# Kernel tuning notes

Measured on AMD Instinct MI355X. Metric: run time of the kernel, lower is better.

The kernel has to match this reference:

```python
import jax, jax.numpy as jnp
import numpy as np

N_NODES = 100000
N_EDGES = 600000
H = 128          # hidden_units
LH = 256         # lin_hidden_units
F_IN = 3         # num_features (x, y, area)
C = 8            # out_classes


def setup_inputs() -> dict:
    key = jax.random.key(0)
    ks = jax.random.split(key, 12)
    s = 0.05
    return {
        "x": jax.random.normal(ks[0], (N_NODES, F_IN), dtype=jnp.float32),
        "edge_index": jax.random.randint(ks[1], (2, N_EDGES), 0, N_NODES, dtype=jnp.int64),
        # conv1: lin_l (aggregated neighbors, has bias), lin_r (root, no bias)
        "Wl1": jax.random.normal(ks[2], (H, F_IN), dtype=jnp.float32) * s,
        "bl1": jnp.zeros((H,), dtype=jnp.float32),
        "Wr1": jax.random.normal(ks[3], (H, F_IN), dtype=jnp.float32) * s,
        # conv2
        "Wl2": jax.random.normal(ks[4], (H, H), dtype=jnp.float32) * s,
        "bl2": jnp.zeros((H,), dtype=jnp.float32),
        "Wr2": jax.random.normal(ks[5], (H, H), dtype=jnp.float32) * s,
        # MLP head
        "W1": jax.random.normal(ks[6], (LH, H), dtype=jnp.float32) * s,
        "b1": jnp.zeros((LH,), dtype=jnp.float32),
        "W2": jax.random.normal(ks[7], (C, LH), dtype=jnp.float32) * s,
        "b2": jnp.zeros((C,), dtype=jnp.float32),
    }


def _normalize(x):
    coords = x[:, :2]                      # [N, 2]
    areas = x[:, 2:3]                      # [N, 1]
    mx = jnp.max(coords, axis=0)
    mn = jnp.min(coords, axis=0)
    theta = jnp.float32(np.pi / 2)
    c, sn = jnp.cos(theta), jnp.sin(theta)
    R = jnp.array([[1.0, 0.0], [0.0, 1.0]], dtype=x.dtype) * c + \
        jnp.array([[0.0, -1.0], [1.0, 0.0]], dtype=x.dtype) * sn
    rotated = coords @ R.T                 # (R @ coords.T).T
    rotate = (mx[1] - mn[1]) > (mx[0] - mn[0])
    coords = jnp.where(rotate, rotated, coords)
    coords = (coords - jnp.mean(coords, axis=0)) / jnp.max(coords, axis=0)
    areas = areas / jnp.max(areas, axis=0)
    return jnp.concatenate([coords, areas], axis=-1)


def _sage_conv(x, src, dst, Wl, bl, Wr):
    # mean aggregation of source features at target nodes
    msg = x[src]                                               # [E, d] gather
    agg = jax.ops.segment_sum(msg, dst, num_segments=N_NODES)  # [N, d]
    deg = jax.ops.segment_sum(jnp.ones((src.shape[0],), x.dtype), dst,
                              num_segments=N_NODES)
    agg = agg / jnp.maximum(deg, 1.0)[:, None]
    return agg @ Wl.T + bl + x @ Wr.T


def reference(x, edge_index, Wl1, bl1, Wr1, Wl2, bl2, Wr2, W1, b1, W2, b2):
    src, dst = edge_index[0], edge_index[1]
    h = _normalize(x)
    h = jnp.tanh(_sage_conv(h, src, dst, Wl1, bl1, Wr1))
    h = jnp.tanh(_sage_conv(h, src, dst, Wl2, bl2, Wr2))
    h = jnp.tanh(h @ W1.T + b1)
    h = h @ W2.T + b2
    return jax.nn.softmax(h, axis=1)
```

## Files before the change

kernel.cpp:

```cpp
#include <hip/hip_runtime.h>
#include <hip/hip_bf16.h>
#include <math.h>

#define N_NODES 100000
#define N_EDGES 600000
#define H 128
#define LH 256
#define CDIM 8
#define NB_STATS 256
#define NT128 ((N_NODES + 127) / 128)
#define ELLW 64
#define NB_NODE ((N_NODES + 255) / 256)

#define NBUCK 391
#define NBLK_P1 64
#define EPB (N_EDGES / NBLK_P1)
#define CAP 72

typedef __attribute__((ext_vector_type(8))) short short8;
typedef __attribute__((ext_vector_type(4))) float floatx4;

#define OFF_PART   0
#define OFF_DEG    2816
#define OFF_H0     (OFF_DEG + N_NODES)
#define OFF_ELL    (OFF_H0 + N_NODES*4)
#define OFF_CNTT   (OFF_ELL + N_NODES*ELLW)
#define OFF_SCR    (OFF_CNTT + NBUCK*NBLK_P1)
#define OFF_WPK2   (OFF_SCR + NBUCK*NBLK_P1*CAP*2)
#define OFF_WPK1   (OFF_WPK2 + 16384)
#define OFF_W2PK   (OFF_WPK1 + 16384)
#define OFF_XB     (OFF_W2PK + 2048)

__device__ __forceinline__ float rot_c() { return cosf(1.57079632679489661923f); }
__device__ __forceinline__ float rot_s() { return sinf(1.57079632679489661923f); }
__device__ __forceinline__ float bfhi(unsigned v) { return __uint_as_float(v & 0xffff0000u); }
__device__ __forceinline__ float bflo(unsigned v) { return __uint_as_float(v << 16); }
__device__ __forceinline__ unsigned short bfu(float f) {
    __hip_bfloat16 h = __float2bfloat16(f);
    return *(unsigned short*)&h;
}
__device__ __forceinline__ float ftanh(float x) {
    float e = __expf(2.0f * x);
    return 1.0f - 2.0f * __builtin_amdgcn_rcpf(e + 1.0f);
}

__global__ __launch_bounds__(256) void statsPart_k(const float* __restrict__ x,
        float* __restrict__ part, const int* __restrict__ ei,
        int* __restrict__ cntT, int2* __restrict__ scratch) {
    __shared__ float red[4][11];
    __shared__ int lcnt[NBUCK];
    int tid = threadIdx.x;

    if (blockIdx.x >= NB_STATS) {
        int blk = blockIdx.x - NB_STATS;
        for (int i = tid; i < NBUCK; i += 256) lcnt[i] = 0;
        __syncthreads();
        int base = blk * EPB;
        for (int e = base + tid; e < base + EPB; e += 256) {
            int s = ei[e], d = ei[N_EDGES + e];
            int b = d >> 8;
            int pos = atomicAdd(&lcnt[b], 1);
            scratch[(b * NBLK_P1 + blk) * CAP + pos] = make_int2(s, d);
        }
        __syncthreads();
        for (int i = tid; i < NBUCK; i += 256)
            cntT[i * NBLK_P1 + blk] = lcnt[i];
        return;
    }

    const float c = rot_c(), sn = rot_s();
    float mn0 = INFINITY, mx0 = -INFINITY, mn1 = INFINITY, mx1 = -INFINITY;
    float s0 = 0.f, s1 = 0.f, sr0 = 0.f, sr1 = 0.f;
    float mxr0 = -INFINITY, mxr1 = -INFINITY, mxa = -INFINITY;
    for (int i = blockIdx.x * 256 + tid; i < N_NODES; i += NB_STATS * 256) {
        float x0 = x[3*i], x1 = x[3*i+1], a = x[3*i+2];
        float r0 = c*x0 - sn*x1;
        float r1 = sn*x0 + c*x1;
        mn0 = fminf(mn0, x0); mx0 = fmaxf(mx0, x0);
        mn1 = fminf(mn1, x1); mx1 = fmaxf(mx1, x1);
        s0 += x0; s1 += x1; sr0 += r0; sr1 += r1;
        mxr0 = fmaxf(mxr0, r0); mxr1 = fmaxf(mxr1, r1);
        mxa = fmaxf(mxa, a);
    }
    float vals[11] = {mn0, mx0, mn1, mx1, s0, s1, sr0, sr1, mxr0, mxr1, mxa};
    int lane = tid & 63, wave = tid >> 6;
    #pragma unroll
    for (int v = 0; v < 11; v++) {
        const int op = (v==0||v==2) ? 0 : (v>=4 && v<=7) ? 2 : 1;
        float val = vals[v];
        #pragma unroll
        for (int off = 32; off > 0; off >>= 1) {
            float o = __shfl_down(val, off);
            val = (op==0) ? fminf(val,o) : (op==1) ? fmaxf(val,o) : (val+o);
        }
        if (lane == 0) red[wave][v] = val;
    }
    __syncthreads();
    if (tid < 11) {
        int v = tid;
        int op = (v==0||v==2) ? 0 : (v>=4 && v<=7) ? 2 : 1;
        float a = red[0][v], b = red[1][v], cc = red[2][v], d = red[3][v];
        float r = (op==0) ? fminf(fminf(a,b), fminf(cc,d))
                : (op==1) ? fmaxf(fmaxf(a,b), fmaxf(cc,d))
                : (a + b + cc + d);
        part[blockIdx.x * 11 + v] = r;
    }
}

__global__ __launch_bounds__(256) void binNorm_k(const float* __restrict__ x,
        const float* __restrict__ part, float4* __restrict__ h0,
        const float* __restrict__ Wl2, const float* __restrict__ Wr2,
        const float* __restrict__ W1, const float* __restrict__ W2,
        __hip_bfloat16* __restrict__ Wpk2, __hip_bfloat16* __restrict__ Wpk1,
        __hip_bfloat16* __restrict__ W2pk,
        const int* __restrict__ cntT, const int2* __restrict__ scratch,
        int* __restrict__ ell, int* __restrict__ deg) {
    __shared__ int pref[NBLK_P1 + 1];
    __shared__ int ncnt[256];
    __shared__ float res[11];
    int tid = threadIdx.x;

    if (blockIdx.x < NBUCK) {
        int b = blockIdx.x;
        ncnt[tid] = 0;
        if (tid < NBLK_P1) pref[tid + 1] = cntT[b * NBLK_P1 + tid];
        __syncthreads();
        if (tid == 0) {
            pref[0] = 0;
            int acc = 0;
            #pragma unroll 8
            for (int j = 0; j < NBLK_P1; j++) { acc += pref[j+1]; pref[j+1] = acc; }
        }
        __syncthreads();
        int T = pref[NBLK_P1];
        for (int f = tid; f < T; f += 256) {
            int lo = 0, hi = NBLK_P1;
            while (hi - lo > 1) {
                int mid = (lo + hi) >> 1;
                if (pref[mid] <= f) lo = mid; else hi = mid;
            }
            int2 sd = scratch[(b * NBLK_P1 + lo) * CAP + (f - pref[lo])];
            int pos = atomicAdd(&ncnt[sd.y & 255], 1);
            ell[(sd.y << 6) + pos] = sd.x;
        }
        __syncthreads();
        int n = (b << 8) + tid;
        if (n < N_NODES) deg[n] = ncnt[tid];
        return;
    }

    int nb = blockIdx.x - NBUCK;
    int i = nb * 256 + tid;
    if (tid < 64) {
        const int ops[11] = {0,1,0,1,2,2,2,2,1,1,1};
        for (int v = 0; v < 11; v++) {
            float val = part[tid * 11 + v];
            #pragma unroll
            for (int p = 1; p < 4; p++) {
                float o = part[(tid + p*64) * 11 + v];
                val = (ops[v]==0) ? fminf(val,o) : (ops[v]==1) ? fmaxf(val,o) : (val+o);
            }
            #pragma unroll
            for (int off = 32; off > 0; off >>= 1) {
                float o = __shfl_down(val, off);
                val = (ops[v]==0) ? fminf(val,o) : (ops[v]==1) ? fmaxf(val,o) : (val+o);
            }
            if (tid == 0) res[v] = val;
        }
    }
    __syncthreads();
    int rotate = (res[3] - res[2]) > (res[1] - res[0]);
    float mean0 = (rotate ? res[6] : res[4]) / (float)N_NODES;
    float mean1 = (rotate ? res[7] : res[5]) / (float)N_NODES;
    float imx0  = 1.0f / (rotate ? res[8] : res[1]);
    float imx1  = 1.0f / (rotate ? res[9] : res[3]);
    float imxa  = 1.0f / res[10];

    if (i < N_NODES) {
        const float c = rot_c(), sn = rot_s();
        float x0 = x[3*i], x1 = x[3*i+1], a = x[3*i+2];
        float u0 = rotate ? (c*x0 - sn*x1) : x0;
        float u1 = rotate ? (sn*x0 + c*x1) : x1;
        h0[i] = make_float4((u0 - mean0) * imx0, (u1 - mean1) * imx1, a * imxa, 0.f);
    }
    int idx = i;
    if (idx < 32768) {
        int j = idx & 7, lane = (idx >> 3) & 63, nt = (idx >> 9) & 7, ks = idx >> 12;
        int k = ks*32 + (lane >> 4)*8 + j;
        int n = nt*16 + (lane & 15);
        float v = (k < 128) ? Wl2[n*H + k] : Wr2[n*H + (k - 128)];
        Wpk2[idx] = __float2bfloat16(v);
    } else if (idx < 65536) {
        int i2 = idx - 32768;
        int j = i2 & 7, lane = (i2 >> 3) & 63, nt = (i2 >> 9) & 15, ks = i2 >> 13;
        int k = ks*32 + (lane >> 4)*8 + j;
        int n = nt*16 + (lane & 15);
        Wpk1[i2] = __float2bfloat16(W1[n*H + k]);
    } else if (idx < 69632) {
        int i3 = idx - 65536;
        int j = i3 & 7, lane = (i3 >> 3) & 63, ks = i3 >> 9;
        int k = ks*32 + (lane >> 4)*8 + j;
        int n = lane & 15;
        W2pk[i3] = __float2bfloat16((n < CDIM) ? W2[n*LH + k] : 0.f);
    }
}

__global__ __launch_bounds__(256) void agg1conv1_k(const float4* __restrict__ h0,
        const int* __restrict__ deg, const int* __restrict__ ell,
        const float* __restrict__ Wl1, const float* __restrict__ bl1,
        const float* __restrict__ Wr1, __hip_bfloat16* __restrict__ Xb) {
    __shared__ float wl[H*3], wr[H*3], bb[H];
    __shared__ float4 sa[256];
    int tid = threadIdx.x;
    for (int i = tid; i < H*3; i += 256) { wl[i] = Wl1[i]; wr[i] = Wr1[i]; }
    if (tid < H) bb[tid] = bl1[tid];
    int base = blockIdx.x * 256;
    int n = base + tid;
    float4 av = make_float4(0.f, 0.f, 0.f, 0.f);
    if (n < N_NODES) {
        int dg = deg[n];
        int start = n << 6, end = start + dg;
        float a0 = 0.f, a1 = 0.f, a2 = 0.f;
        int e = start;
        for (; e + 3 < end; e += 4) {
            int s0 = ell[e], s1 = ell[e+1], s2 = ell[e+2], s3 = ell[e+3];
            float4 v0 = h0[s0];
            float4 v1 = h0[s1];
            float4 v2 = h0[s2];
            float4 v3 = h0[s3];
            a0 += (v0.x + v1.x) + (v2.x + v3.x);
            a1 += (v0.y + v1.y) + (v2.y + v3.y);
            a2 += (v0.z + v1.z) + (v2.z + v3.z);
        }
        for (; e < end; e++) {
            float4 v = h0[ell[e]];
            a0 += v.x; a1 += v.y; a2 += v.z;
        }
        float inv = 1.0f / (float)max(dg, 1);
        av = make_float4(a0 * inv, a1 * inv, a2 * inv, 0.f);
    }
    sa[tid] = av;
    __syncthreads();
    int sub = tid >> 6;
    int j2 = (tid & 63) * 2;
    for (int i = 0; i < 64; i++) {
        int loc = i * 4 + sub;
        int nn = base + loc;
        if (nn >= N_NODES) break;
        float4 a = sa[loc];
        float4 xv = h0[nn];
        float o0 = wl[3*j2+0]*a.x + wl[3*j2+1]*a.y + wl[3*j2+2]*a.z + bb[j2]
                 + wr[3*j2+0]*xv.x + wr[3*j2+1]*xv.y + wr[3*j2+2]*xv.z;
        float o1 = wl[3*j2+3]*a.x + wl[3*j2+4]*a.y + wl[3*j2+5]*a.z + bb[j2+1]
                 + wr[3*j2+3]*xv.x + wr[3*j2+4]*xv.y + wr[3*j2+5]*xv.z;
        unsigned pv = ((unsigned)bfu(ftanh(o1)) << 16) | (unsigned)bfu(ftanh(o0));
        *(unsigned*)&Xb[(size_t)nn*256 + 128 + j2] = pv;
    }
}

__global__ void agg2_k(__hip_bfloat16* __restrict__ Xb, const int* __restrict__ deg,
                       const int* __restrict__ ell) {
    int lane = threadIdx.x & 15;
    int n = blockIdx.x * 16 + (threadIdx.x >> 4);
    int dg = deg[n];
    int start = n << 6, end = start + dg;
    const short* XbS = (const short*)Xb;
    float a0=0.f,a1=0.f,a2=0.f,a3=0.f,a4=0.f,a5=0.f,a6=0.f,a7=0.f;
    int e = start;
    for (; e + 1 < end; e += 2) {
        int s0 = ell[e], s1 = ell[e+1];
        uint4 v0 = *(const uint4*)&XbS[(size_t)s0*256 + 128 + lane*8];
        uint4 v1 = *(const uint4*)&XbS[(size_t)s1*256 + 128 + lane*8];
        a0 += bflo(v0.x) + bflo(v1.x); a1 += bfhi(v0.x) + bfhi(v1.x);
        a2 += bflo(v0.y) + bflo(v1.y); a3 += bfhi(v0.y) + bfhi(v1.y);
        a4 += bflo(v0.z) + bflo(v1.z); a5 += bfhi(v0.z) + bfhi(v1.z);
        a6 += bflo(v0.w) + bflo(v1.w); a7 += bfhi(v0.w) + bfhi(v1.w);
    }
    if (e < end) {
        int s0 = ell[e];
        uint4 v0 = *(const uint4*)&XbS[(size_t)s0*256 + 128 + lane*8];
        a0 += bflo(v0.x); a1 += bfhi(v0.x);
        a2 += bflo(v0.y); a3 += bfhi(v0.y);
        a4 += bflo(v0.z); a5 += bfhi(v0.z);
        a6 += bflo(v0.w); a7 += bfhi(v0.w);
    }
    float inv = 1.0f / (float)max(dg, 1);
    uint4 o;
    o.x = ((unsigned)bfu(a1*inv) << 16) | (unsigned)bfu(a0*inv);
    o.y = ((unsigned)bfu(a3*inv) << 16) | (unsigned)bfu(a2*inv);
    o.z = ((unsigned)bfu(a5*inv) << 16) | (unsigned)bfu(a4*inv);
    o.w = ((unsigned)bfu(a7*inv) << 16) | (unsigned)bfu(a6*inv);
    *(uint4*)&Xb[(size_t)n*256 + lane*8] = o;
}

__global__ __launch_bounds__(512, 1) void conv2mlp_k(const __hip_bfloat16* __restrict__ Xb,
        const __hip_bfloat16* __restrict__ Wpk2, const float* __restrict__ bl2,
        const __hip_bfloat16* __restrict__ Wpk1, const float* __restrict__ b1,
        const __hip_bfloat16* __restrict__ W2pk, const float* __restrict__ b2,
        float* __restrict__ out) {
    __shared__ short Ws2[32768];
    __shared__ short Ws1[32768];
    __shared__ short Cs[8 * 16 * 128];
    int tid = threadIdx.x;
    int lane = tid & 63, wave = tid >> 6;
    int quad = lane >> 4, m = lane & 15, c0 = lane & 15;
    {
        const float4* s2 = (const float4*)Wpk2;
        const float4* s1 = (const float4*)Wpk1;
        float4* d2 = (float4*)Ws2;
        float4* d1 = (float4*)Ws1;
        #pragma unroll
        for (int i = 0; i < 8; i++) {
            d2[tid + i*512] = s2[tid + i*512];
            d1[tid + i*512] = s1[tid + i*512];
        }
    }
    short8 w2f[8];
    #pragma unroll
    for (int ks = 0; ks < 8; ks++)
        w2f[ks] = *(const short8*)&W2pk[(ks*64 + lane)*8];
    float bl2r[8], b1r[16];
    #pragma unroll
    for (int nt = 0; nt < 8; nt++) bl2r[nt] = bl2[nt*16 + c0];
    #pragma unroll
    for (int nt = 0; nt < 16; nt++) b1r[nt] = b1[nt*16 + c0];
    float b2v = (c0 < CDIM) ? b2[c0] : 0.f;
    __syncthreads();
    short* Tw = &Cs[wave * (16 * 128)];

    int tile = blockIdx.x;
    short8 areg[8];
    {
        int row = tile*128 + wave*16 + m;
        int rowL = row < N_NODES ? row : N_NODES - 1;
        const short* Arow = (const short*)Xb + (size_t)rowL * 256;
        #pragma unroll
        for (int ks = 0; ks < 8; ks++)
            areg[ks] = *(const short8*)(Arow + ks*32 + quad*8);
    }
    for (; tile < NT128; tile += gridDim.x) {
        short8 anext[8];
        {
            int tnext = tile + gridDim.x;
            int rown = (tnext < NT128) ? (tnext*128 + wave*16 + m) : 0;
            int rowNL = rown < N_NODES ? rown : N_NODES - 1;
            const short* ArowN = (const short*)Xb + (size_t)rowNL * 256;
            #pragma unroll
            for (int ks = 0; ks < 8; ks++)
                anext[ks] = *(const short8*)(ArowN + ks*32 + quad*8);
        }
        floatx4 acc2[8];
        #pragma unroll
        for (int i = 0; i < 8; i++)
            #pragma unroll
            for (int r = 0; r < 4; r++) acc2[i][r] = 0.f;
        #pragma unroll
        for (int ks = 0; ks < 8; ks++) {
            #pragma unroll
            for (int nt = 0; nt < 8; nt++) {
                short8 b = *(const short8*)&Ws2[((ks*8 + nt)*64 + lane)*8];
                acc2[nt] = __builtin_amdgcn_mfma_f32_16x16x32_bf16(areg[ks], b, acc2[nt], 0, 0, 0);
            }
        }
        #pragma unroll
        for (int nt = 0; nt < 8; nt++) {
            int cg = nt*2 + (c0 >> 3);
            #pragma unroll
            for (int r = 0; r < 4; r++) {
                int row = quad*4 + r;
                Tw[row*128 + ((cg ^ row) << 3) + (c0 & 7)] =
                    (short)bfu(ftanh(acc2[nt][r] + bl2r[nt]));
            }
        }
        floatx4 acc1[16];
        #pragma unroll
        for (int i = 0; i < 16; i++)
            #pragma unroll
            for (int r = 0; r < 4; r++) acc1[i][r] = 0.f;
        #pragma unroll
        for (int ks = 0; ks < 4; ks++) {
            short8 a = *(const short8*)&Tw[m*128 + (((ks*4 + quad) ^ m) << 3)];
            #pragma unroll
            for (int nt = 0; nt < 16; nt++) {
                short8 b = *(const short8*)&Ws1[((ks*16 + nt)*64 + lane)*8];
                acc1[nt] = __builtin_amdgcn_mfma_f32_16x16x32_bf16(a, b, acc1[nt], 0, 0, 0);
            }
        }
        floatx4 lacc;
        #pragma unroll
        for (int r = 0; r < 4; r++) lacc[r] = 0.f;
        #pragma unroll
        for (int ch = 0; ch < 4; ch++) {
            #pragma unroll
            for (int ntl = 0; ntl < 4; ntl++) {
                int nt = ch*4 + ntl;
                int cg = ntl*2 + (c0 >> 3);
                #pragma unroll
                for (int r = 0; r < 4; r++) {
                    int row = quad*4 + r;
                    Tw[row*128 + ((cg ^ row) << 3) + (c0 & 7)] =
                        (short)bfu(ftanh(acc1[nt][r] + b1r[nt]));
                }
            }
            #pragma unroll
            for (int k2 = 0; k2 < 2; k2++) {
                short8 a = *(const short8*)&Tw[m*128 + (((k2*4 + quad) ^ m) << 3)];
                lacc = __builtin_amdgcn_mfma_f32_16x16x32_bf16(a, w2f[ch*2 + k2], lacc, 0, 0, 0);
            }
        }
        int rbase = tile*128 + wave*16 + quad*4;
        #pragma unroll
        for (int r = 0; r < 4; r++) {
            float v = lacc[r] + b2v;
            float mval = (c0 < CDIM) ? v : -INFINITY;
            #pragma unroll
            for (int off = 1; off < 8; off <<= 1)
                mval = fmaxf(mval, __shfl_xor(mval, off));
            float e = (c0 < CDIM) ? __expf(v - mval) : 0.f;
            float ssum = e;
            #pragma unroll
            for (int off = 1; off < 8; off <<= 1)
                ssum += __shfl_xor(ssum, off);
            int rowg = rbase + r;
            if (c0 < CDIM && rowg < N_NODES)
                out[(size_t)rowg*CDIM + c0] = e / ssum;
        }
        #pragma unroll
        for (int ks = 0; ks < 8; ks++) areg[ks] = anext[ks];
    }
}

extern "C" void kernel_launch(void* const* d_in, const int* in_sizes, int n_in,
                              void* d_out, int out_size, void* d_ws, size_t ws_size,
                              hipStream_t stream) {
    const float* x   = (const float*)d_in[0];
    const int*   ei  = (const int*)d_in[1];
    const float* Wl1 = (const float*)d_in[2];
    const float* bl1 = (const float*)d_in[3];
    const float* Wr1 = (const float*)d_in[4];
    const float* Wl2 = (const float*)d_in[5];
    const float* bl2 = (const float*)d_in[6];
    const float* Wr2 = (const float*)d_in[7];
    const float* W1  = (const float*)d_in[8];
    const float* b1  = (const float*)d_in[9];
    const float* W2  = (const float*)d_in[10];
    const float* b2  = (const float*)d_in[11];

    float* ws     = (float*)d_ws;
    float* part   = ws + OFF_PART;
    int*   deg    = (int*)(ws + OFF_DEG);
    float4* h0    = (float4*)(ws + OFF_H0);
    int*   ell    = (int*)(ws + OFF_ELL);
    int*   cntT   = (int*)(ws + OFF_CNTT);
    int2*  scratch= (int2*)(ws + OFF_SCR);
    __hip_bfloat16* Wpk2 = (__hip_bfloat16*)(ws + OFF_WPK2);
    __hip_bfloat16* Wpk1 = (__hip_bfloat16*)(ws + OFF_WPK1);
    __hip_bfloat16* W2pk = (__hip_bfloat16*)(ws + OFF_W2PK);
    __hip_bfloat16* Xb   = (__hip_bfloat16*)(ws + OFF_XB);

    statsPart_k<<<NB_STATS + NBLK_P1, 256, 0, stream>>>(x, part, ei, cntT, scratch);
    binNorm_k<<<NBUCK + NB_NODE, 256, 0, stream>>>(x, part, h0,
            Wl2, Wr2, W1, W2, Wpk2, Wpk1, W2pk, cntT, scratch, ell, deg);
    agg1conv1_k<<<NB_NODE, 256, 0, stream>>>(h0, deg, ell,
            Wl1, bl1, Wr1, Xb);
    agg2_k<<<N_NODES / 16, 256, 0, stream>>>(Xb, deg, ell);
    conv2mlp_k<<<256, 512, 0, stream>>>(Xb, Wpk2, bl2, Wpk1, b1, W2pk, b2,
            (float*)d_out);
}
```

Before: 206.2 us.

## Drop LDS weight staging and persistent loop in conv2+MLP kernel

Instead of a persistent grid of 256 blocks that first copy both packed weight matrices into shared memory, the kernel now launches one block per 128-row tile. B fragments are read straight from global memory through the cache, and launch bounds allow up to 4 blocks per CU. This removes the 128 KB LDS footprint and the per-block staging prologue, which should raise occupancy and hide latency with more waves. The cost is repeated global/L2 weight loads per tile and the loss of the next-tile prefetch.

```diff
diff --git a/kernel.cpp b/kernel.cpp
--- a/kernel.cpp
+++ b/kernel.cpp
@@ -293,40 +293,19 @@
     *(uint4*)&Xb[(size_t)n*256 + lane*8] = o;
 }
 
-__global__ __launch_bounds__(512, 1) void conv2mlp_k(const __hip_bfloat16* __restrict__ Xb,
+__global__ __launch_bounds__(512, 4) void conv2mlp_k(const __hip_bfloat16* __restrict__ Xb,
         const __hip_bfloat16* __restrict__ Wpk2, const float* __restrict__ bl2,
         const __hip_bfloat16* __restrict__ Wpk1, const float* __restrict__ b1,
         const __hip_bfloat16* __restrict__ W2pk, const float* __restrict__ b2,
         float* __restrict__ out) {
-    __shared__ short Ws2[32768];
-    __shared__ short Ws1[32768];
     __shared__ short Cs[8 * 16 * 128];
     int tid = threadIdx.x;
     int lane = tid & 63, wave = tid >> 6;
     int quad = lane >> 4, m = lane & 15, c0 = lane & 15;
-    {
-        const float4* s2 = (const float4*)Wpk2;
-        const float4* s1 = (const float4*)Wpk1;
-        float4* d2 = (float4*)Ws2;
-        float4* d1 = (float4*)Ws1;
-        #pragma unroll
-        for (int i = 0; i < 8; i++) {
-            d2[tid + i*512] = s2[tid + i*512];
-            d1[tid + i*512] = s1[tid + i*512];
-        }
-    }
-    short8 w2f[8];
-    #pragma unroll
-    for (int ks = 0; ks < 8; ks++)
-        w2f[ks] = *(const short8*)&W2pk[(ks*64 + lane)*8];
-    float bl2r[8], b1r[16];
-    #pragma unroll
-    for (int nt = 0; nt < 8; nt++) bl2r[nt] = bl2[nt*16 + c0];
-    #pragma unroll
-    for (int nt = 0; nt < 16; nt++) b1r[nt] = b1[nt*16 + c0];
-    float b2v = (c0 < CDIM) ? b2[c0] : 0.f;
-    __syncthreads();
     short* Tw = &Cs[wave * (16 * 128)];
+    const short* Bg2 = (const short*)Wpk2;
+    const short* Bg1 = (const short*)Wpk1;
+    const short* Bg0 = (const short*)W2pk;
 
     int tile = blockIdx.x;
     short8 areg[8];
@@ -338,95 +317,85 @@
         for (int ks = 0; ks < 8; ks++)
             areg[ks] = *(const short8*)(Arow + ks*32 + quad*8);
     }
-    for (; tile < NT128; tile += gridDim.x) {
-        short8 anext[8];
-        {
-            int tnext = tile + gridDim.x;
-            int rown = (tnext < NT128) ? (tnext*128 + wave*16 + m) : 0;
-            int rowNL = rown < N_NODES ? rown : N_NODES - 1;
-            const short* ArowN = (const short*)Xb + (size_t)rowNL * 256;
-            #pragma unroll
-            for (int ks = 0; ks < 8; ks++)
-                anext[ks] = *(const short8*)(ArowN + ks*32 + quad*8);
-        }
-        floatx4 acc2[8];
-        #pragma unroll
-        for (int i = 0; i < 8; i++)
-            #pragma unroll
-            for (int r = 0; r < 4; r++) acc2[i][r] = 0.f;
-        #pragma unroll
-        for (int ks = 0; ks < 8; ks++) {
-            #pragma unroll
-            for (int nt = 0; nt < 8; nt++) {
-                short8 b = *(const short8*)&Ws2[((ks*8 + nt)*64 + lane)*8];
-                acc2[nt] = __builtin_amdgcn_mfma_f32_16x16x32_bf16(areg[ks], b, acc2[nt], 0, 0, 0);
-            }
-        }
+    floatx4 acc2[8];
+    #pragma unroll
+    for (int i = 0; i < 8; i++)
+        #pragma unroll
+        for (int r = 0; r < 4; r++) acc2[i][r] = 0.f;
+    #pragma unroll
+    for (int ks = 0; ks < 8; ks++) {
         #pragma unroll
         for (int nt = 0; nt < 8; nt++) {
-            int cg = nt*2 + (c0 >> 3);
+            short8 b = *(const short8*)&Bg2[((ks*8 + nt)*64 + lane)*8];
+            acc2[nt] = __builtin_amdgcn_mfma_f32_16x16x32_bf16(areg[ks], b, acc2[nt], 0, 0, 0);
+        }
+    }
+    #pragma unroll
+    for (int nt = 0; nt < 8; nt++) {
+        float bl2v = bl2[nt*16 + c0];
+        int cg = nt*2 + (c0 >> 3);
+        #pragma unroll
+        for (int r = 0; r < 4; r++) {
+            int row = quad*4 + r;
+            Tw[row*128 + ((cg ^ row) << 3) + (c0 & 7)] =
+                (short)bfu(ftanh(acc2[nt][r] + bl2v));
+        }
+    }
+    floatx4 acc1[16];
+    #pragma unroll
+    for (int i = 0; i < 16; i++)
+        #pragma unroll
+        for (int r = 0; r < 4; r++) acc1[i][r] = 0.f;
+    #pragma unroll
+    for (int ks = 0; ks < 4; ks++) {
+        short8 a = *(const short8*)&Tw[m*128 + (((ks*4 + quad) ^ m) << 3)];
+        #pragma unroll
+        for (int nt = 0; nt < 16; nt++) {
+            short8 b = *(const short8*)&Bg1[((ks*16 + nt)*64 + lane)*8];
+            acc1[nt] = __builtin_amdgcn_mfma_f32_16x16x32_bf16(a, b, acc1[nt], 0, 0, 0);
+        }
+    }
+    floatx4 lacc;
+    #pragma unroll
+    for (int r = 0; r < 4; r++) lacc[r] = 0.f;
+    #pragma unroll
+    for (int ch = 0; ch < 4; ch++) {
+        #pragma unroll
+        for (int ntl = 0; ntl < 4; ntl++) {
+            int nt = ch*4 + ntl;
+            float b1v = b1[nt*16 + c0];
+            int cg = ntl*2 + (c0 >> 3);
             #pragma unroll
             for (int r = 0; r < 4; r++) {
                 int row = quad*4 + r;
                 Tw[row*128 + ((cg ^ row) << 3) + (c0 & 7)] =
-                    (short)bfu(ftanh(acc2[nt][r] + bl2r[nt]));
+                    (short)bfu(ftanh(acc1[nt][r] + b1v));
             }
         }
-        floatx4 acc1[16];
-        #pragma unroll
-        for (int i = 0; i < 16; i++)
-            #pragma unroll
-            for (int r = 0; r < 4; r++) acc1[i][r] = 0.f;
-        #pragma unroll
-        for (int ks = 0; ks < 4; ks++) {
-            short8 a = *(const short8*)&Tw[m*128 + (((ks*4 + quad) ^ m) << 3)];
-            #pragma unroll
-            for (int nt = 0; nt < 16; nt++) {
-                short8 b = *(const short8*)&Ws1[((ks*16 + nt)*64 + lane)*8];
-                acc1[nt] = __builtin_amdgcn_mfma_f32_16x16x32_bf16(a, b, acc1[nt], 0, 0, 0);
-            }
-        }
-        floatx4 lacc;
-        #pragma unroll
-        for (int r = 0; r < 4; r++) lacc[r] = 0.f;
-        #pragma unroll
-        for (int ch = 0; ch < 4; ch++) {
-            #pragma unroll
-            for (int ntl = 0; ntl < 4; ntl++) {
-                int nt = ch*4 + ntl;
-                int cg = ntl*2 + (c0 >> 3);
-                #pragma unroll
-                for (int r = 0; r < 4; r++) {
-                    int row = quad*4 + r;
-                    Tw[row*128 + ((cg ^ row) << 3) + (c0 & 7)] =
-                        (short)bfu(ftanh(acc1[nt][r] + b1r[nt]));
-                }
-            }
-            #pragma unroll
-            for (int k2 = 0; k2 < 2; k2++) {
-                short8 a = *(const short8*)&Tw[m*128 + (((k2*4 + quad) ^ m) << 3)];
-                lacc = __builtin_amdgcn_mfma_f32_16x16x32_bf16(a, w2f[ch*2 + k2], lacc, 0, 0, 0);
-            }
-        }
-        int rbase = tile*128 + wave*16 + quad*4;
-        #pragma unroll
-        for (int r = 0; r < 4; r++) {
-            float v = lacc[r] + b2v;
-            float mval = (c0 < CDIM) ? v : -INFINITY;
-            #pragma unroll
-            for (int off = 1; off < 8; off <<= 1)
-                mval = fmaxf(mval, __shfl_xor(mval, off));
-            float e = (c0 < CDIM) ? __expf(v - mval) : 0.f;
-            float ssum = e;
-            #pragma unroll
-            for (int off = 1; off < 8; off <<= 1)
-                ssum += __shfl_xor(ssum, off);
-            int rowg = rbase + r;
-            if (c0 < CDIM && rowg < N_NODES)
-                out[(size_t)rowg*CDIM + c0] = e / ssum;
-        }
-        #pragma unroll
-        for (int ks = 0; ks < 8; ks++) areg[ks] = anext[ks];
+        #pragma unroll
+        for (int k2 = 0; k2 < 2; k2++) {
+            short8 a = *(const short8*)&Tw[m*128 + (((k2*4 + quad) ^ m) << 3)];
+            short8 w2 = *(const short8*)&Bg0[((ch*2 + k2)*64 + lane)*8];
+            lacc = __builtin_amdgcn_mfma_f32_16x16x32_bf16(a, w2, lacc, 0, 0, 0);
+        }
+    }
+    float b2v = (c0 < CDIM) ? b2[c0] : 0.f;
+    int rbase = tile*128 + wave*16 + quad*4;
+    #pragma unroll
+    for (int r = 0; r < 4; r++) {
+        float v = lacc[r] + b2v;
+        float mval = (c0 < CDIM) ? v : -INFINITY;
+        #pragma unroll
+        for (int off = 1; off < 8; off <<= 1)
+            mval = fmaxf(mval, __shfl_xor(mval, off));
+        float e = (c0 < CDIM) ? __expf(v - mval) : 0.f;
+        float ssum = e;
+        #pragma unroll
+        for (int off = 1; off < 8; off <<= 1)
+            ssum += __shfl_xor(ssum, off);
+        int rowg = rbase + r;
+        if (c0 < CDIM && rowg < N_NODES)
+            out[(size_t)rowg*CDIM + c0] = e / ssum;
     }
 }
 
@@ -464,6 +433,6 @@
     agg1conv1_k<<<NB_NODE, 256, 0, stream>>>(h0, deg, ell,
             Wl1, bl1, Wr1, Xb);
     agg2_k<<<N_NODES / 16, 256, 0, stream>>>(Xb, deg, ell);
-    conv2mlp_k<<<256, 512, 0, stream>>>(Xb, Wpk2, bl2, Wpk1, b1, W2pk, b2,
+    conv2mlp_k<<<NT128, 512, 0, stream>>>(Xb, Wpk2, bl2, Wpk1, b1, W2pk, b2,
             (float*)d_out);
 }
```

Measured after the change: 219.5 us. +6.5%, slower.

## Fuse second-layer neighbor aggregation into conv2+MLP kernel, one tile per block

Applied to the files above, without the earlier changes.

Removes the separate agg2 kernel. Each conv2mlp block now gathers neighbor features for its own 128 rows in registers and converts them straight into MFMA A-fragments, so the aggregated bf16 half of Xb is no longer written to and re-read from global memory. The grid changes from a persistent 256-block loop to one block per 128-row tile (782 blocks). In exchange, the gather's latency now sits inside a kernel that runs at low occupancy (512 threads, 1 block per CU, large LDS) and that reloads 128 KB of weights per block. The inter-tile prefetch of A rows is also dropped.

```diff
diff --git a/kernel.cpp b/kernel.cpp
--- a/kernel.cpp
+++ b/kernel.cpp
@@ -35,6 +35,9 @@
 __device__ __forceinline__ float rot_s() { return sinf(1.57079632679489661923f); }
 __device__ __forceinline__ float bfhi(unsigned v) { return __uint_as_float(v & 0xffff0000u); }
 __device__ __forceinline__ float bflo(unsigned v) { return __uint_as_float(v << 16); }
+__device__ __forceinline__ float bfs(short s) {
+    return __uint_as_float(((unsigned)(unsigned short)s) << 16);
+}
 __device__ __forceinline__ unsigned short bfu(float f) {
     __hip_bfloat16 h = __float2bfloat16(f);
     return *(unsigned short*)&h;
@@ -258,42 +261,8 @@
     }
 }
 
-__global__ void agg2_k(__hip_bfloat16* __restrict__ Xb, const int* __restrict__ deg,
-                       const int* __restrict__ ell) {
-    int lane = threadIdx.x & 15;
-    int n = blockIdx.x * 16 + (threadIdx.x >> 4);
-    int dg = deg[n];
-    int start = n << 6, end = start + dg;
-    const short* XbS = (const short*)Xb;
-    float a0=0.f,a1=0.f,a2=0.f,a3=0.f,a4=0.f,a5=0.f,a6=0.f,a7=0.f;
-    int e = start;
-    for (; e + 1 < end; e += 2) {
-        int s0 = ell[e], s1 = ell[e+1];
-        uint4 v0 = *(const uint4*)&XbS[(size_t)s0*256 + 128 + lane*8];
-        uint4 v1 = *(const uint4*)&XbS[(size_t)s1*256 + 128 + lane*8];
-        a0 += bflo(v0.x) + bflo(v1.x); a1 += bfhi(v0.x) + bfhi(v1.x);
-        a2 += bflo(v0.y) + bflo(v1.y); a3 += bfhi(v0.y) + bfhi(v1.y);
-        a4 += bflo(v0.z) + bflo(v1.z); a5 += bfhi(v0.z) + bfhi(v1.z);
-        a6 += bflo(v0.w) + bflo(v1.w); a7 += bfhi(v0.w) + bfhi(v1.w);
-    }
-    if (e < end) {
-        int s0 = ell[e];
-        uint4 v0 = *(const uint4*)&XbS[(size_t)s0*256 + 128 + lane*8];
-        a0 += bflo(v0.x); a1 += bfhi(v0.x);
-        a2 += bflo(v0.y); a3 += bfhi(v0.y);
-        a4 += bflo(v0.z); a5 += bfhi(v0.z);
-        a6 += bflo(v0.w); a7 += bfhi(v0.w);
-    }
-    float inv = 1.0f / (float)max(dg, 1);
-    uint4 o;
-    o.x = ((unsigned)bfu(a1*inv) << 16) | (unsigned)bfu(a0*inv);
-    o.y = ((unsigned)bfu(a3*inv) << 16) | (unsigned)bfu(a2*inv);
-    o.z = ((unsigned)bfu(a5*inv) << 16) | (unsigned)bfu(a4*inv);
-    o.w = ((unsigned)bfu(a7*inv) << 16) | (unsigned)bfu(a6*inv);
-    *(uint4*)&Xb[(size_t)n*256 + lane*8] = o;
-}
-
 __global__ __launch_bounds__(512, 1) void conv2mlp_k(const __hip_bfloat16* __restrict__ Xb,
+        const int* __restrict__ deg, const int* __restrict__ ell,
         const __hip_bfloat16* __restrict__ Wpk2, const float* __restrict__ bl2,
         const __hip_bfloat16* __restrict__ Wpk1, const float* __restrict__ b1,
         const __hip_bfloat16* __restrict__ W2pk, const float* __restrict__ b2,
@@ -325,108 +294,135 @@
     #pragma unroll
     for (int nt = 0; nt < 16; nt++) b1r[nt] = b1[nt*16 + c0];
     float b2v = (c0 < CDIM) ? b2[c0] : 0.f;
+
+    int tile = blockIdx.x;
+    int row = tile*128 + wave*16 + m;
+    int rowL = row < N_NODES ? row : N_NODES - 1;
+    const short* XbS = (const short*)Xb;
+    int dg = deg[rowL];
+    int estart = rowL << 6;
+    float ga[32];
+    #pragma unroll
+    for (int i = 0; i < 32; i++) ga[i] = 0.f;
+    int e = 0;
+    for (; e + 1 < dg; e += 2) {
+        int s0 = ell[estart + e], s1 = ell[estart + e + 1];
+        const short* p0 = XbS + (size_t)s0*256 + 128 + quad*8;
+        const short* p1 = XbS + (size_t)s1*256 + 128 + quad*8;
+        #pragma unroll
+        for (int ks = 0; ks < 4; ks++) {
+            short8 v0 = *(const short8*)(p0 + ks*32);
+            short8 v1 = *(const short8*)(p1 + ks*32);
+            #pragma unroll
+            for (int j = 0; j < 8; j++)
+                ga[ks*8+j] += bfs(v0[j]) + bfs(v1[j]);
+        }
+    }
+    if (e < dg) {
+        int s0 = ell[estart + e];
+        const short* p0 = XbS + (size_t)s0*256 + 128 + quad*8;
+        #pragma unroll
+        for (int ks = 0; ks < 4; ks++) {
+            short8 v0 = *(const short8*)(p0 + ks*32);
+            #pragma unroll
+            for (int j = 0; j < 8; j++)
+                ga[ks*8+j] += bfs(v0[j]);
+        }
+    }
+    short8 areg[8];
+    {
+        float inv = 1.0f / (float)max(dg, 1);
+        #pragma unroll
+        for (int ks = 0; ks < 4; ks++) {
+            short8 t;
+            #pragma unroll
+            for (int j = 0; j < 8; j++)
+                t[j] = (short)bfu(ga[ks*8+j] * inv);
+            areg[ks] = t;
+        }
+        const short* Arow = XbS + (size_t)rowL * 256;
+        #pragma unroll
+        for (int ks = 4; ks < 8; ks++)
+            areg[ks] = *(const short8*)(Arow + ks*32 + quad*8);
+    }
     __syncthreads();
     short* Tw = &Cs[wave * (16 * 128)];
 
-    int tile = blockIdx.x;
-    short8 areg[8];
-    {
-        int row = tile*128 + wave*16 + m;
-        int rowL = row < N_NODES ? row : N_NODES - 1;
-        const short* Arow = (const short*)Xb + (size_t)rowL * 256;
-        #pragma unroll
-        for (int ks = 0; ks < 8; ks++)
-            areg[ks] = *(const short8*)(Arow + ks*32 + quad*8);
-    }
-    for (; tile < NT128; tile += gridDim.x) {
-        short8 anext[8];
-        {
-            int tnext = tile + gridDim.x;
-            int rown = (tnext < NT128) ? (tnext*128 + wave*16 + m) : 0;
-            int rowNL = rown < N_NODES ? rown : N_NODES - 1;
-            const short* ArowN = (const short*)Xb + (size_t)rowNL * 256;
-            #pragma unroll
-            for (int ks = 0; ks < 8; ks++)
-                anext[ks] = *(const short8*)(ArowN + ks*32 + quad*8);
-        }
-        floatx4 acc2[8];
-        #pragma unroll
-        for (int i = 0; i < 8; i++)
-            #pragma unroll
-            for (int r = 0; r < 4; r++) acc2[i][r] = 0.f;
-        #pragma unroll
-        for (int ks = 0; ks < 8; ks++) {
-            #pragma unroll
-            for (int nt = 0; nt < 8; nt++) {
-                short8 b = *(const short8*)&Ws2[((ks*8 + nt)*64 + lane)*8];
-                acc2[nt] = __builtin_amdgcn_mfma_f32_16x16x32_bf16(areg[ks], b, acc2[nt], 0, 0, 0);
+    floatx4 acc2[8];
+    #pragma unroll
+    for (int i = 0; i < 8; i++)
+        #pragma unroll
+        for (int r = 0; r < 4; r++) acc2[i][r] = 0.f;
+    #pragma unroll
+    for (int ks = 0; ks < 8; ks++) {
+        #pragma unroll
+        for (int nt = 0; nt < 8; nt++) {
+            short8 b = *(const short8*)&Ws2[((ks*8 + nt)*64 + lane)*8];
+            acc2[nt] = __builtin_amdgcn_mfma_f32_16x16x32_bf16(areg[ks], b, acc2[nt], 0, 0, 0);
+        }
+    }
+    #pragma unroll
+    for (int nt = 0; nt < 8; nt++) {
+        int cg = nt*2 + (c0 >> 3);
+        #pragma unroll
+        for (int r = 0; r < 4; r++) {
+            int row2 = quad*4 + r;
+            Tw[row2*128 + ((cg ^ row2) << 3) + (c0 & 7)] =
+                (short)bfu(ftanh(acc2[nt][r] + bl2r[nt]));
+        }
+    }
+    floatx4 acc1[16];
+    #pragma unroll
+    for (int i = 0; i < 16; i++)
+        #pragma unroll
+        for (int r = 0; r < 4; r++) acc1[i][r] = 0.f;
+    #pragma unroll
+    for (int ks = 0; ks < 4; ks++) {
+        short8 a = *(const short8*)&Tw[m*128 + (((ks*4 + quad) ^ m) << 3)];
+        #pragma unroll
+        for (int nt = 0; nt < 16; nt++) {
+            short8 b = *(const short8*)&Ws1[((ks*16 + nt)*64 + lane)*8];
+            acc1[nt] = __builtin_amdgcn_mfma_f32_16x16x32_bf16(a, b, acc1[nt], 0, 0, 0);
+        }
+    }
+    floatx4 lacc;
+    #pragma unroll
+    for (int r = 0; r < 4; r++) lacc[r] = 0.f;
+    #pragma unroll
+    for (int ch = 0; ch < 4; ch++) {
+        #pragma unroll
+        for (int ntl = 0; ntl < 4; ntl++) {
+            int nt = ch*4 + ntl;
+            int cg = ntl*2 + (c0 >> 3);
+            #pragma unroll
+            for (int r = 0; r < 4; r++) {
+                int row2 = quad*4 + r;
+                Tw[row2*128 + ((cg ^ row2) << 3) + (c0 & 7)] =
+                    (short)bfu(ftanh(acc1[nt][r] + b1r[nt]));
             }
         }
         #pragma unroll
-        for (int nt = 0; nt < 8; nt++) {
-            int cg = nt*2 + (c0 >> 3);
-            #pragma unroll
-            for (int r = 0; r < 4; r++) {
-                int row = quad*4 + r;
-                Tw[row*128 + ((cg ^ row) << 3) + (c0 & 7)] =
-                    (short)bfu(ftanh(acc2[nt][r] + bl2r[nt]));
-            }
-        }
-        floatx4 acc1[16];
-        #pragma unroll
-        for (int i = 0; i < 16; i++)
-            #pragma unroll
-            for (int r = 0; r < 4; r++) acc1[i][r] = 0.f;
-        #pragma unroll
-        for (int ks = 0; ks < 4; ks++) {
-            short8 a = *(const short8*)&Tw[m*128 + (((ks*4 + quad) ^ m) << 3)];
-            #pragma unroll
-            for (int nt = 0; nt < 16; nt++) {
-                short8 b = *(const short8*)&Ws1[((ks*16 + nt)*64 + lane)*8];
-                acc1[nt] = __builtin_amdgcn_mfma_f32_16x16x32_bf16(a, b, acc1[nt], 0, 0, 0);
-            }
-        }
-        floatx4 lacc;
-        #pragma unroll
-        for (int r = 0; r < 4; r++) lacc[r] = 0.f;
-        #pragma unroll
-        for (int ch = 0; ch < 4; ch++) {
-            #pragma unroll
-            for (int ntl = 0; ntl < 4; ntl++) {
-                int nt = ch*4 + ntl;
-                int cg = ntl*2 + (c0 >> 3);
-                #pragma unroll
-                for (int r = 0; r < 4; r++) {
-                    int row = quad*4 + r;
-                    Tw[row*128 + ((cg ^ row) << 3) + (c0 & 7)] =
-                        (short)bfu(ftanh(acc1[nt][r] + b1r[nt]));
-                }
-            }
-            #pragma unroll
-            for (int k2 = 0; k2 < 2; k2++) {
-                short8 a = *(const short8*)&Tw[m*128 + (((k2*4 + quad) ^ m) << 3)];
-                lacc = __builtin_amdgcn_mfma_f32_16x16x32_bf16(a, w2f[ch*2 + k2], lacc, 0, 0, 0);
-            }
-        }
-        int rbase = tile*128 + wave*16 + quad*4;
-        #pragma unroll
-        for (int r = 0; r < 4; r++) {
-            float v = lacc[r] + b2v;
-            float mval = (c0 < CDIM) ? v : -INFINITY;
-            #pragma unroll
-            for (int off = 1; off < 8; off <<= 1)
-                mval = fmaxf(mval, __shfl_xor(mval, off));
-            float e = (c0 < CDIM) ? __expf(v - mval) : 0.f;
-            float ssum = e;
-            #pragma unroll
-            for (int off = 1; off < 8; off <<= 1)
-                ssum += __shfl_xor(ssum, off);
-            int rowg = rbase + r;
-            if (c0 < CDIM && rowg < N_NODES)
-                out[(size_t)rowg*CDIM + c0] = e / ssum;
-        }
-        #pragma unroll
-        for (int ks = 0; ks < 8; ks++) areg[ks] = anext[ks];
+        for (int k2 = 0; k2 < 2; k2++) {
+            short8 a = *(const short8*)&Tw[m*128 + (((k2*4 + quad) ^ m) << 3)];
+            lacc = __builtin_amdgcn_mfma_f32_16x16x32_bf16(a, w2f[ch*2 + k2], lacc, 0, 0, 0);
+        }
+    }
+    int rbase = tile*128 + wave*16 + quad*4;
+    #pragma unroll
+    for (int r = 0; r < 4; r++) {
+        float v = lacc[r] + b2v;
+        float mval = (c0 < CDIM) ? v : -INFINITY;
+        #pragma unroll
+        for (int off = 1; off < 8; off <<= 1)
+            mval = fmaxf(mval, __shfl_xor(mval, off));
+        float e2 = (c0 < CDIM) ? __expf(v - mval) : 0.f;
+        float ssum = e2;
+        #pragma unroll
+        for (int off = 1; off < 8; off <<= 1)
+            ssum += __shfl_xor(ssum, off);
+        int rowg = rbase + r;
+        if (c0 < CDIM && rowg < N_NODES)
+            out[(size_t)rowg*CDIM + c0] = e2 / ssum;
     }
 }
 
@@ -463,7 +459,6 @@
             Wl2, Wr2, W1, W2, Wpk2, Wpk1, W2pk, cntT, scratch, ell, deg);
     agg1conv1_k<<<NB_NODE, 256, 0, stream>>>(h0, deg, ell,
             Wl1, bl1, Wr1, Xb);
-    agg2_k<<<N_NODES / 16, 256, 0, stream>>>(Xb, deg, ell);
-    conv2mlp_k<<<256, 512, 0, stream>>>(Xb, Wpk2, bl2, Wpk1, b1, W2pk, b2,
-            (float*)d_out);
-}
+    conv2mlp_k<<<NT128, 512, 0, stream>>>(Xb, deg, ell, Wpk2, bl2, Wpk1, b1,
+            W2pk, b2, (float*)d_out);
+}
```

Measured after the change: 210.6 us. 1.02x slower.
